# Performance work log

Hardware: AMD Instinct MI355X
Metric: run time of the kernel (lower is better)

## Reference

```python
import jax, jax.numpy as jnp
import numpy as np

B, S, E, H = 4, 2048, 2048, 16
D = E // H  # 128


def _rope(x, sin, cos):
    # x: (B, S, H, D); sin/cos: (S, D//2)
    x1, x2 = jnp.split(x, 2, axis=-1)
    c = cos[None, :, None, :]
    s = sin[None, :, None, :]
    return jnp.concatenate([x1 * c - x2 * s, x1 * s + x2 * c], axis=-1)


def setup_inputs() -> dict:
    key = jax.random.key(0)
    ks = jax.random.split(key, 12)
    inp = {
        "x_q": jax.random.normal(ks[0], (B, S, E), jnp.float32),
        "x_kv": jax.random.normal(ks[1], (B, S, E), jnp.float32),
        "Wq": jax.random.normal(ks[2], (E, E), jnp.float32) / np.sqrt(E),
        "bq": jnp.zeros((E,), jnp.float32),
        "Wk": jax.random.normal(ks[3], (E, E), jnp.float32) / np.sqrt(E),
        "bk": jnp.zeros((E,), jnp.float32),
        "Wv": jax.random.normal(ks[4], (E, E), jnp.float32) / np.sqrt(E),
        "bv": jnp.zeros((E,), jnp.float32),
        "Wo": jax.random.normal(ks[5], (E, E), jnp.float32) / np.sqrt(E),
        "bo": jnp.zeros((E,), jnp.float32),
        "angles": jax.random.uniform(ks[6], (2, S, D // 2), jnp.float32),
        "attn_mask": jnp.ones((B, S), jnp.int32),
        "causal": 0,
        "k_rope": 1,
    }
    return inp


def reference(x_q, x_kv, Wq, bq, Wk, bk, Wv, bv, Wo, bo, angles, attn_mask, causal, k_rope):
    sin, cos = angles[0], angles[1]
    q = (x_q @ Wq.T + bq).reshape(B, S, H, D)
    k = (x_kv @ Wk.T + bk).reshape(B, S, H, D)
    v = (x_kv @ Wv.T + bv).reshape(B, S, H, D)
    q = _rope(q, sin, cos)
    if k_rope:
        k = _rope(k, sin, cos)
    # scaled dot-product attention, heads leading: (B, H, S, S)
    scores = jnp.einsum("bqhd,bkhd->bhqk", q, k) / np.sqrt(D).astype(np.float32)
    mask = attn_mask.astype(bool)[:, None, None, :]  # (B,1,1,S_kv)
    if causal:
        cm = jnp.tril(jnp.ones((S, S), bool))[None, None]
        mask = mask & cm
    scores = jnp.where(mask, scores, jnp.finfo(scores.dtype).min)
    probs = jax.nn.softmax(scores, axis=-1)
    attn = jnp.einsum("bhqk,bkhd->bqhd", probs, v).reshape(B, S, E)
    return attn @ Wo.T + bo
```

## Files before the change

### kernel.cpp

```cpp
#include <hip/hip_runtime.h>
#include <hip/hip_bf16.h>


typedef __bf16 bf16;
typedef __bf16 bf16x8 __attribute__((ext_vector_type(8)));
typedef __bf16 bf16x4 __attribute__((ext_vector_type(4)));
typedef __bf16 bf16x2 __attribute__((ext_vector_type(2)));
typedef float  f32x4  __attribute__((ext_vector_type(4)));
typedef float  f32x16 __attribute__((ext_vector_type(16)));

constexpr int Bc = 4, Sc = 2048, Ec = 2048, Hc = 16, Dc = 128;
constexpr int Mc = Bc * Sc;

__device__ __forceinline__ void async16(const void* g, void* l) {
  __builtin_amdgcn_global_load_lds(
      (const __attribute__((address_space(1))) void*)g,
      (__attribute__((address_space(3))) void*)l, 16, 0, 0);
}

__device__ __forceinline__ unsigned int pkbf(float a, float b) {
  union { bf16x2 v; unsigned int u; } c;
  c.v[0] = (bf16)a; c.v[1] = (bf16)b;
  return c.u;
}

__device__ __forceinline__ int swzb32(int r, int kb) {
  int b = r * 64 + kb;
  return b ^ (((b >> 9) & 1) << 5);
}

__global__ void cvt_kernel(const float* __restrict__ src, bf16* __restrict__ dst, int n8) {
  int i = blockIdx.x * blockDim.x + threadIdx.x;
  const int stride = gridDim.x * blockDim.x;
  for (; i < n8; i += stride) {
    const float4 a = *((const float4*)src + (size_t)i * 2);
    const float4 b = *((const float4*)src + (size_t)i * 2 + 1);
    bf16x8 o;
    o[0] = (bf16)a.x; o[1] = (bf16)a.y; o[2] = (bf16)a.z; o[3] = (bf16)a.w;
    o[4] = (bf16)b.x; o[5] = (bf16)b.y; o[6] = (bf16)b.z; o[7] = (bf16)b.w;
    *(bf16x8*)(dst + (size_t)i * 8) = o;
  }
}

template <int OUT_BF16>
__global__ __launch_bounds__(512, 2) void gemm8(
    const bf16* __restrict__ A, const bf16* __restrict__ Bm,
    const float* __restrict__ bias, void* __restrict__ Cout, int Mblocks)
{
  __shared__ __align__(16) bf16 lds[3 * 16384];
  const int tid = threadIdx.x;
  const int w = tid >> 6, lane = tid & 63;
  const int l15 = lane & 15, l16 = lane >> 4;
  const int wm = w >> 2, wn = w & 3;
  const int id = blockIdx.x;
  const int nwg = Mblocks * 8, cpx = nwg >> 3;
  const int swz = (id & 7) * cpx + (id >> 3);
  const int by = swz >> 3, bx = swz & 7;
  const long m0 = (long)by * 256, n0 = (long)bx * 256;
  constexpr int NT = 64;

  auto stA = [&](int buf, long kt, int j) {
    int c = w * 128 + j * 64 + lane;
    int cs = c ^ (((c >> 5) & 1) << 1);
    async16(A + (m0 + (cs >> 2)) * 2048 + kt + (cs & 3) * 8,
            &lds[buf * 16384 + c * 8]);
  };
  auto stB = [&](int buf, long kt, int j) {
    int c = w * 128 + j * 64 + lane;
    int cs = c ^ (((c >> 5) & 1) << 1);
    async16(Bm + (n0 + (cs >> 2)) * 2048 + kt + (cs & 3) * 8,
            &lds[buf * 16384 + 8192 + c * 8]);
  };

  f32x4 acc[8][4];
#pragma unroll
  for (int a = 0; a < 8; ++a)
#pragma unroll
    for (int b = 0; b < 4; ++b) acc[a][b] = f32x4{0.f, 0.f, 0.f, 0.f};

  stA(0, 0, 0); stA(0, 0, 1); stB(0, 0, 0); stB(0, 0, 1);
  stA(1, 32, 0); stA(1, 32, 1); stB(1, 32, 0); stB(1, 32, 1);
  asm volatile("s_waitcnt vmcnt(4)" ::: "memory");
  __builtin_amdgcn_s_barrier();

  int cur = 0, nx = 2;
  for (int t = 0; t < NT; ++t) {
    const char* Ab = (const char*)&lds[cur * 16384];
    const char* Bb = Ab + 16384;
    const long ktn = (long)(t + 2) * 32;
    const bool pf = (t < NT - 2);

    bf16x8 af[8], bf0[2];
#pragma unroll
    for (int mf = 0; mf < 8; ++mf)
      af[mf] = *(const bf16x8*)(Ab + swzb32(wm * 128 + mf * 16 + l15, l16 * 16));
#pragma unroll
    for (int nf = 0; nf < 2; ++nf)
      bf0[nf] = *(const bf16x8*)(Bb + swzb32(wn * 64 + nf * 16 + l15, l16 * 16));
    if (pf) { stA(nx, ktn, 0); stA(nx, ktn, 1); }
    asm volatile("" ::: "memory");
    __builtin_amdgcn_s_barrier();
    __builtin_amdgcn_s_setprio(1);
#pragma unroll
    for (int mf = 0; mf < 8; ++mf)
#pragma unroll
      for (int nf = 0; nf < 2; ++nf)
        acc[mf][nf] = __builtin_amdgcn_mfma_f32_16x16x32_bf16(af[mf], bf0[nf], acc[mf][nf], 0, 0, 0);
    __builtin_amdgcn_s_setprio(0);
    __builtin_amdgcn_s_barrier();

    bf16x8 bf1[2];
#pragma unroll
    for (int nf = 0; nf < 2; ++nf)
      bf1[nf] = *(const bf16x8*)(Bb + swzb32(wn * 64 + (2 + nf) * 16 + l15, l16 * 16));
    if (pf) { stB(nx, ktn, 0); stB(nx, ktn, 1); }
    asm volatile("" ::: "memory");
    __builtin_amdgcn_s_barrier();
    __builtin_amdgcn_s_setprio(1);
#pragma unroll
    for (int mf = 0; mf < 8; ++mf)
#pragma unroll
      for (int nf = 0; nf < 2; ++nf)
        acc[mf][2 + nf] = __builtin_amdgcn_mfma_f32_16x16x32_bf16(af[mf], bf1[nf], acc[mf][2 + nf], 0, 0, 0);
    __builtin_amdgcn_s_setprio(0);
    if (t < NT - 2)       { asm volatile("s_waitcnt vmcnt(4)" ::: "memory"); }
    else if (t == NT - 2) { asm volatile("s_waitcnt vmcnt(0)" ::: "memory"); }
    __builtin_amdgcn_s_barrier();
    cur = (cur == 2) ? 0 : cur + 1;
    nx  = (nx  == 2) ? 0 : nx  + 1;
  }

#pragma unroll
  for (int mf = 0; mf < 8; ++mf)
#pragma unroll
    for (int nf = 0; nf < 4; ++nf) {
      const long m = m0 + wm * 128 + mf * 16 + l16 * 4;
      const long n = n0 + wn * 64 + nf * 16 + l15;
      const float bv = bias[n];
#pragma unroll
      for (int i = 0; i < 4; ++i) {
        float v = acc[mf][nf][i] + bv;
        if (OUT_BF16) ((bf16*)Cout)[(m + i) * 2048 + n] = (bf16)v;
        else          ((float*)Cout)[(m + i) * 2048 + n] = v;
      }
    }
}

__global__ void rope_kernel(bf16* __restrict__ x, const float* __restrict__ angles,
                            const int* __restrict__ flag, int force)
{
  if (!force && flag[0] == 0) return;
  const int t = threadIdx.x;
  const long R = (long)blockIdx.x * 64 + (t >> 2);
  const int d0 = (t & 3) * 16;
  const long s = (R / Hc) % Sc;
  bf16* rowp = x + R * Dc;
  bf16x8 lo0 = *(bf16x8*)(rowp + d0);
  bf16x8 lo1 = *(bf16x8*)(rowp + d0 + 8);
  bf16x8 hi0 = *(bf16x8*)(rowp + d0 + 64);
  bf16x8 hi1 = *(bf16x8*)(rowp + d0 + 72);
  const float* sp = angles + s * 64 + d0;
  const float* cp = angles + 131072 + s * 64 + d0;
  bf16x8 a0, a1, b0, b1;
#pragma unroll
  for (int j = 0; j < 8; ++j) {
    float c = cp[j], sn = sp[j];
    float x1 = (float)lo0[j], x2 = (float)hi0[j];
    a0[j] = (bf16)(x1 * c - x2 * sn);
    b0[j] = (bf16)(x1 * sn + x2 * c);
    float c1 = cp[j + 8], sn1 = sp[j + 8];
    float y1 = (float)lo1[j], y2 = (float)hi1[j];
    a1[j] = (bf16)(y1 * c1 - y2 * sn1);
    b1[j] = (bf16)(y1 * sn1 + y2 * c1);
  }
  *(bf16x8*)(rowp + d0)      = a0;
  *(bf16x8*)(rowp + d0 + 8)  = a1;
  *(bf16x8*)(rowp + d0 + 64) = b0;
  *(bf16x8*)(rowp + d0 + 72) = b1;
}

__global__ void transpose_v(const bf16* __restrict__ v0, bf16* __restrict__ Vt)
{
  __shared__ __align__(16) bf16 T[64 * 128];
  const int t = threadIdx.x;
  const int bh = blockIdx.y, b = bh >> 4, h = bh & 15;
  const int s0 = blockIdx.x * 64;
#pragma unroll
  for (int it = 0; it < 4; ++it) {
    int slot = it * 256 + t;
    int r = slot >> 4, g = slot & 15;
    async16(v0 + ((size_t)(b * Sc + s0 + r) * Hc + h) * Dc + ((g ^ (r & 15)) << 3),
            &T[slot * 8]);
  }
  __syncthreads();
  const int d = t >> 1, half = t & 1;
  bf16x8 pk[4];
#pragma unroll
  for (int j = 0; j < 32; ++j) {
    int sl = half * 32 + j;
    pk[j >> 3][j & 7] = T[sl * 128 + (((d >> 3) ^ (sl & 15)) << 3) + (d & 7)];
  }
  bf16* op = Vt + ((size_t)bh * Dc + d) * Sc + s0 + half * 32;
#pragma unroll
  for (int v = 0; v < 4; ++v) *(bf16x8*)(op + v * 8) = pk[v];
}

__global__ __launch_bounds__(256, 2) void attn_kernel(
    const bf16* __restrict__ q0, const bf16* __restrict__ k0,
    const bf16* __restrict__ vt, const int* __restrict__ mask,
    const int* __restrict__ causal_p, bf16* __restrict__ attn_out)
{
  __shared__ __align__(16) bf16 Ks[2][64 * 128];
  __shared__ __align__(16) bf16 Vs[2][128 * 64];

  const int tid = threadIdx.x, wid = tid >> 6, lane = tid & 63;
  const int l31 = lane & 31, h = lane >> 5;
  const int id = blockIdx.x;
  const int swz = (id & 7) * 128 + (id >> 3);
  const int bh = swz >> 4, qb = swz & 15;
  const int b = bh >> 4, hh = bh & 15;
  const int q_glob = qb * 128 + wid * 32 + l31;
  const int causal_f = causal_p[0];
  const float SC = 0.08838834764831845f * 1.4426950408889634f;
  const float NEG = -3.0e38f;

  auto stageKV = [&](int kv0s, int bufs) {
#pragma unroll
    for (int it = 0; it < 4; ++it) {
      int g = it * 256 + tid;
      int r = g >> 4, gp = g & 15;
      async16(k0 + ((size_t)(b * Sc + kv0s + r) * Hc + hh) * Dc + ((gp ^ (r & 15)) << 3),
              &Ks[bufs][g * 8]);
    }
#pragma unroll
    for (int it = 0; it < 4; ++it) {
      int g = it * 256 + tid;
      int r = g >> 3, gp = g & 7;
      async16(vt + ((size_t)bh * Dc + r) * Sc + kv0s + ((gp ^ (r & 7)) << 3),
              &Vs[bufs][g * 8]);
    }
  };

  bf16x8 qf[8];
#pragma unroll
  for (int dc = 0; dc < 8; ++dc)
    qf[dc] = *(const bf16x8*)(q0 + ((size_t)(b * Sc + q_glob) * Hc + hh) * Dc + dc * 16 + h * 8);

  f32x16 o[4];
#pragma unroll
  for (int db = 0; db < 4; ++db)
#pragma unroll
    for (int r = 0; r < 16; ++r) o[db][r] = 0.f;
  float mrun = NEG, lrun = 0.f;

  stageKV(0, 0);
  asm volatile("s_waitcnt vmcnt(0)" ::: "memory");
  __builtin_amdgcn_s_barrier();
  int cur = 0;

  for (int kv0 = 0; kv0 < Sc; kv0 += 64) {
    if (kv0 + 64 < Sc) stageKV(kv0 + 64, cur ^ 1);
    const unsigned long long mbits = __ballot(mask[b * Sc + kv0 + lane] != 0);

#pragma unroll
    for (int kvb = 0; kvb < 2; ++kvb) {
      f32x16 s;
#pragma unroll
      for (int r = 0; r < 16; ++r) s[r] = 0.f;
      __builtin_amdgcn_s_setprio(1);
#pragma unroll
      for (int dc = 0; dc < 8; ++dc) {
        bf16x8 kf = *(const bf16x8*)&Ks[cur][(kvb * 32 + l31) * 128 +
                                           (((dc * 2 + h) ^ (l31 & 15)) << 3)];
        s = __builtin_amdgcn_mfma_f32_32x32x16_bf16(kf, qf[dc], s, 0, 0, 0);
      }
      __builtin_amdgcn_s_setprio(0);
#pragma unroll
      for (int r = 0; r < 16; ++r) s[r] *= SC;
      if (mbits != ~0ull) {
#pragma unroll
        for (int r = 0; r < 16; ++r) {
          int off = kvb * 32 + (r & 3) + 8 * (r >> 2) + 4 * h;
          if (!((mbits >> off) & 1)) s[r] = NEG;
        }
      }
      if (causal_f) {
#pragma unroll
        for (int r = 0; r < 16; ++r) {
          int kvg = kv0 + kvb * 32 + (r & 3) + 8 * (r >> 2) + 4 * h;
          if (kvg > q_glob) s[r] = NEG;
        }
      }
      float tmax = s[0];
#pragma unroll
      for (int r = 1; r < 16; ++r) tmax = fmaxf(tmax, s[r]);
      tmax = fmaxf(tmax, __shfl_xor(tmax, 32));
      if (!__all(tmax <= mrun + 8.0f)) {
        const float mnew = fmaxf(mrun, tmax);
        const float alpha = __builtin_amdgcn_exp2f(mrun - mnew);
#pragma unroll
        for (int db = 0; db < 4; ++db)
#pragma unroll
          for (int r = 0; r < 16; ++r) o[db][r] *= alpha;
        lrun *= alpha;
        mrun = mnew;
      }
      float rs = 0.f;
#pragma unroll
      for (int r = 0; r < 16; ++r) {
        s[r] = __builtin_amdgcn_exp2f(s[r] - mrun);
        rs += s[r];
      }
      rs += __shfl_xor(rs, 32);
      lrun += rs;
      unsigned int dw0 = pkbf(s[0], s[1]),   dw1 = pkbf(s[2], s[3]);
      unsigned int dw2 = pkbf(s[4], s[5]),   dw3 = pkbf(s[6], s[7]);
      unsigned int dw4 = pkbf(s[8], s[9]),   dw5 = pkbf(s[10], s[11]);
      unsigned int dw6 = pkbf(s[12], s[13]), dw7 = pkbf(s[14], s[15]);
      asm volatile("v_permlane32_swap_b32 %0, %1" : "+v"(dw0), "+v"(dw2));
      asm volatile("v_permlane32_swap_b32 %0, %1" : "+v"(dw1), "+v"(dw3));
      asm volatile("v_permlane32_swap_b32 %0, %1" : "+v"(dw4), "+v"(dw6));
      asm volatile("v_permlane32_swap_b32 %0, %1" : "+v"(dw5), "+v"(dw7));
      union { unsigned int u[4]; bf16x8 v; } pf0, pf1;
      pf0.u[0] = dw0; pf0.u[1] = dw1; pf0.u[2] = dw2; pf0.u[3] = dw3;
      pf1.u[0] = dw4; pf1.u[1] = dw5; pf1.u[2] = dw6; pf1.u[3] = dw7;
      __builtin_amdgcn_s_setprio(1);
#pragma unroll
      for (int ksb = 0; ksb < 2; ++ksb) {
        const bf16x8 pfv = ksb ? pf1.v : pf0.v;
#pragma unroll
        for (int db = 0; db < 4; ++db) {
          const int dr = db * 32 + l31;
          bf16x8 vb = *(const bf16x8*)&Vs[cur][dr * 64 +
                          ((((kvb * 2 + ksb) * 2 + h) ^ (dr & 7)) << 3)];
          o[db] = __builtin_amdgcn_mfma_f32_32x32x16_bf16(vb, pfv, o[db], 0, 0, 0);
        }
      }
      __builtin_amdgcn_s_setprio(0);
    }
    asm volatile("s_waitcnt vmcnt(0)" ::: "memory");
    __builtin_amdgcn_s_barrier();
    cur ^= 1;
  }

  const float inv = 1.0f / lrun;
  bf16* orow = attn_out + ((size_t)(b * Sc + q_glob) * Hc + hh) * Dc;
#pragma unroll
  for (int db = 0; db < 4; ++db)
#pragma unroll
    for (int rq = 0; rq < 4; ++rq) {
      bf16x4 st;
#pragma unroll
      for (int i = 0; i < 4; ++i) st[i] = (bf16)(o[db][rq * 4 + i] * inv);
      *(bf16x4*)(orow + db * 32 + rq * 8 + 4 * h) = st;
    }
}

extern "C" void kernel_launch(void* const* d_in, const int* in_sizes, int n_in,
                              void* d_out, int out_size, void* d_ws, size_t ws_size,
                              hipStream_t stream)
{
  const float* x_q    = (const float*)d_in[0];
  const float* x_kv   = (const float*)d_in[1];
  const float* Wq     = (const float*)d_in[2];
  const float* bq     = (const float*)d_in[3];
  const float* Wk     = (const float*)d_in[4];
  const float* bk     = (const float*)d_in[5];
  const float* Wv     = (const float*)d_in[6];
  const float* bv     = (const float*)d_in[7];
  const float* Wo     = (const float*)d_in[8];
  const float* bo     = (const float*)d_in[9];
  const float* angles = (const float*)d_in[10];
  const int*   amask  = (const int*)d_in[11];
  const int*   causal = (const int*)d_in[12];
  const int*   k_rope = (const int*)d_in[13];
  float* out = (float*)d_out;

  char* ws = (char*)d_ws;
  const size_t MB32 = (size_t)33554432;
  bf16* xq16  = (bf16*)(ws);
  bf16* xkv16 = (bf16*)(ws + MB32);
  bf16* wq16  = (bf16*)(ws + 2 * MB32);
  bf16* wk16  = wq16 + 4194304;
  bf16* wv16  = wk16 + 4194304;
  bf16* wo16  = wv16 + 4194304;
  bf16* q0    = (bf16*)(ws + 3 * MB32);
  bf16* k0    = (bf16*)(ws + 4 * MB32);
  bf16* v0    = (bf16*)(ws + 5 * MB32);
  bf16* Vt     = xq16;
  bf16* attn16 = xkv16;

  cvt_kernel<<<2048, 256, 0, stream>>>(x_q,  xq16,  Mc * Ec / 8);
  cvt_kernel<<<2048, 256, 0, stream>>>(x_kv, xkv16, Mc * Ec / 8);
  cvt_kernel<<<2048, 256, 0, stream>>>(Wq, wq16, Ec * Ec / 8);
  cvt_kernel<<<2048, 256, 0, stream>>>(Wk, wk16, Ec * Ec / 8);
  cvt_kernel<<<2048, 256, 0, stream>>>(Wv, wv16, Ec * Ec / 8);
  cvt_kernel<<<2048, 256, 0, stream>>>(Wo, wo16, Ec * Ec / 8);

  const int gemmBlocks = (Mc / 256) * (Ec / 256);
  gemm8<1><<<gemmBlocks, 512, 0, stream>>>(xq16,  wq16, bq, q0, Mc / 256);
  gemm8<1><<<gemmBlocks, 512, 0, stream>>>(xkv16, wk16, bk, k0, Mc / 256);
  gemm8<1><<<gemmBlocks, 512, 0, stream>>>(xkv16, wv16, bv, v0, Mc / 256);

  rope_kernel<<<2048, 256, 0, stream>>>(q0, angles, k_rope, 1);
  rope_kernel<<<2048, 256, 0, stream>>>(k0, angles, k_rope, 0);
  transpose_v<<<dim3(Sc / 64, Bc * Hc), 256, 0, stream>>>(v0, Vt);

  attn_kernel<<<1024, 256, 0, stream>>>(q0, k0, Vt, amask, causal, attn16);

  gemm8<0><<<gemmBlocks, 512, 0, stream>>>(attn16, wo16, bo, out, Mc / 256);
}
```

Before: 545.4 us.

## Fuse Q RoPE into attention, batch conversions, and double attention block size

New measurement: 737.5 us. 1.35x slower.

```diff
diff --git a/kernel.cpp b/kernel.cpp
--- a/kernel.cpp
+++ b/kernel.cpp
@@ -29,7 +29,15 @@
   return b ^ (((b >> 9) & 1) << 5);
 }
 
-__global__ void cvt_kernel(const float* __restrict__ src, bf16* __restrict__ dst, int n8) {
+__global__ void cvt_multi(const float* s0, const float* s1, const float* s2, const float* s3,
+                          bf16* d0, bf16* d1, bf16* d2, bf16* d3, int n8) {
+  const float* src; bf16* dst;
+  switch (blockIdx.y) {
+    case 0:  src = s0; dst = d0; break;
+    case 1:  src = s1; dst = d1; break;
+    case 2:  src = s2; dst = d2; break;
+    default: src = s3; dst = d3; break;
+  }
   int i = blockIdx.x * blockDim.x + threadIdx.x;
   const int stride = gridDim.x * blockDim.x;
   for (; i < n8; i += stride) {
@@ -205,10 +213,11 @@
   for (int v = 0; v < 4; ++v) *(bf16x8*)(op + v * 8) = pk[v];
 }
 
-__global__ __launch_bounds__(256, 2) void attn_kernel(
+__global__ __launch_bounds__(512, 4) void attn_kernel(
     const bf16* __restrict__ q0, const bf16* __restrict__ k0,
     const bf16* __restrict__ vt, const int* __restrict__ mask,
-    const int* __restrict__ causal_p, bf16* __restrict__ attn_out)
+    const int* __restrict__ causal_p, const float* __restrict__ angles,
+    bf16* __restrict__ attn_out)
 {
   __shared__ __align__(16) bf16 Ks[2][64 * 128];
   __shared__ __align__(16) bf16 Vs[2][128 * 64];
@@ -216,25 +225,25 @@
   const int tid = threadIdx.x, wid = tid >> 6, lane = tid & 63;
   const int l31 = lane & 31, h = lane >> 5;
   const int id = blockIdx.x;
-  const int swz = (id & 7) * 128 + (id >> 3);
-  const int bh = swz >> 4, qb = swz & 15;
+  const int swz = (id & 7) * 64 + (id >> 3);
+  const int bh = swz >> 3, qb = swz & 7;
   const int b = bh >> 4, hh = bh & 15;
-  const int q_glob = qb * 128 + wid * 32 + l31;
+  const int q_glob = qb * 256 + wid * 32 + l31;
   const int causal_f = causal_p[0];
   const float SC = 0.08838834764831845f * 1.4426950408889634f;
   const float NEG = -3.0e38f;
 
   auto stageKV = [&](int kv0s, int bufs) {
 #pragma unroll
-    for (int it = 0; it < 4; ++it) {
-      int g = it * 256 + tid;
+    for (int it = 0; it < 2; ++it) {
+      int g = it * 512 + tid;
       int r = g >> 4, gp = g & 15;
       async16(k0 + ((size_t)(b * Sc + kv0s + r) * Hc + hh) * Dc + ((gp ^ (r & 15)) << 3),
               &Ks[bufs][g * 8]);
     }
 #pragma unroll
-    for (int it = 0; it < 4; ++it) {
-      int g = it * 256 + tid;
+    for (int it = 0; it < 2; ++it) {
+      int g = it * 512 + tid;
       int r = g >> 3, gp = g & 7;
       async16(vt + ((size_t)bh * Dc + r) * Sc + kv0s + ((gp ^ (r & 7)) << 3),
               &Vs[bufs][g * 8]);
@@ -242,9 +251,26 @@
   };
 
   bf16x8 qf[8];
-#pragma unroll
-  for (int dc = 0; dc < 8; ++dc)
-    qf[dc] = *(const bf16x8*)(q0 + ((size_t)(b * Sc + q_glob) * Hc + hh) * Dc + dc * 16 + h * 8);
+  {
+    const bf16* qrow = q0 + ((size_t)(b * Sc + q_glob) * Hc + hh) * Dc;
+#pragma unroll
+    for (int dc = 0; dc < 4; ++dc) {
+      bf16x8 lo = *(const bf16x8*)(qrow + dc * 16 + h * 8);
+      bf16x8 hi = *(const bf16x8*)(qrow + (dc + 4) * 16 + h * 8);
+      const float* sp = angles + (size_t)q_glob * 64 + dc * 16 + h * 8;
+      union { float4 v[2]; float f[8]; } sn, cs;
+      sn.v[0] = ((const float4*)sp)[0];
+      sn.v[1] = ((const float4*)sp)[1];
+      cs.v[0] = ((const float4*)(sp + 131072))[0];
+      cs.v[1] = ((const float4*)(sp + 131072))[1];
+#pragma unroll
+      for (int j = 0; j < 8; ++j) {
+        float x1 = (float)lo[j], x2 = (float)hi[j];
+        qf[dc][j]     = (bf16)(x1 * cs.f[j] - x2 * sn.f[j]);
+        qf[dc + 4][j] = (bf16)(x1 * sn.f[j] + x2 * cs.f[j]);
+      }
+    }
+  }
 
   f32x16 o[4];
 #pragma unroll
@@ -390,23 +416,20 @@
   bf16* Vt     = xq16;
   bf16* attn16 = xkv16;
 
-  cvt_kernel<<<2048, 256, 0, stream>>>(x_q,  xq16,  Mc * Ec / 8);
-  cvt_kernel<<<2048, 256, 0, stream>>>(x_kv, xkv16, Mc * Ec / 8);
-  cvt_kernel<<<2048, 256, 0, stream>>>(Wq, wq16, Ec * Ec / 8);
-  cvt_kernel<<<2048, 256, 0, stream>>>(Wk, wk16, Ec * Ec / 8);
-  cvt_kernel<<<2048, 256, 0, stream>>>(Wv, wv16, Ec * Ec / 8);
-  cvt_kernel<<<2048, 256, 0, stream>>>(Wo, wo16, Ec * Ec / 8);
+  cvt_multi<<<dim3(1024, 2), 256, 0, stream>>>(x_q, x_kv, x_q, x_kv,
+                                               xq16, xkv16, xq16, xkv16, Mc * Ec / 8);
+  cvt_multi<<<dim3(256, 4), 256, 0, stream>>>(Wq, Wk, Wv, Wo,
+                                              wq16, wk16, wv16, wo16, Ec * Ec / 8);
 
   const int gemmBlocks = (Mc / 256) * (Ec / 256);
   gemm8<1><<<gemmBlocks, 512, 0, stream>>>(xq16,  wq16, bq, q0, Mc / 256);
   gemm8<1><<<gemmBlocks, 512, 0, stream>>>(xkv16, wk16, bk, k0, Mc / 256);
   gemm8<1><<<gemmBlocks, 512, 0, stream>>>(xkv16, wv16, bv, v0, Mc / 256);
 
-  rope_kernel<<<2048, 256, 0, stream>>>(q0, angles, k_rope, 1);
   rope_kernel<<<2048, 256, 0, stream>>>(k0, angles, k_rope, 0);
   transpose_v<<<dim3(Sc / 64, Bc * Hc), 256, 0, stream>>>(v0, Vt);
 
-  attn_kernel<<<1024, 256, 0, stream>>>(q0, k0, Vt, amask, causal, attn16);
+  attn_kernel<<<512, 512, 0, stream>>>(q0, k0, Vt, amask, causal, angles, attn16);
 
   gemm8<0><<<gemmBlocks, 512, 0, stream>>>(attn16, wo16, bo, out, Mc / 256);
 }
```
